# Performance work log

Measured on AMD Instinct MI355X. Metric: run time of the kernel, lower is better.

The kernel has to match this reference:

```python
import jax, jax.numpy as jnp
import numpy as np

B, L, D = 2, 2048, 1024
H, DH = 16, 64            # heads, dim_head; inner_dim = H*DH = 1024
SCALE = DH ** -0.5


def setup_inputs() -> dict:
    key = jax.random.key(0)
    ks = jax.random.split(key, 7)
    s = 0.02
    return {
        "x": jax.random.normal(ks[0], (B, L, D), dtype=jnp.float32),
        "attention_mask": jnp.zeros((B * H, L, L), dtype=jnp.float32),
        "Wq": jax.random.normal(ks[1], (H * DH, D), dtype=jnp.float32) * s,
        "Wk": jax.random.normal(ks[2], (H * DH, D), dtype=jnp.float32) * s,
        "Wv": jax.random.normal(ks[3], (H * DH, D), dtype=jnp.float32) * s,
        "Wo": jax.random.normal(ks[4], (D, H * DH), dtype=jnp.float32) * s,
        "bo": jnp.zeros((D,), dtype=jnp.float32),
    }


def _split_heads(t):
    # [B, L, H*DH] -> [(B*H), L, DH]
    b, l, _ = t.shape
    return t.reshape(b, l, H, DH).transpose(0, 2, 1, 3).reshape(b * H, l, DH)


def reference(x, attention_mask, Wq, Wk, Wv, Wo, bo):
    # Self-attention: encoder_hidden_states = hidden_states
    q = _split_heads(jnp.einsum('bld,ed->ble', x, Wq))  # [(B*H), L, DH]
    k = _split_heads(jnp.einsum('bld,ed->ble', x, Wk))
    v = _split_heads(jnp.einsum('bld,ed->ble', x, Wv))
    # baddbmm: mask + scale * q @ k^T  -> [(B*H), L, L]
    scores = attention_mask + SCALE * jnp.einsum('nqd,nkd->nqk', q, k)
    probs = jax.nn.softmax(scores, axis=-1)
    hidden = jnp.einsum('nqk,nkd->nqd', probs, v)       # [(B*H), L, DH]
    hidden = hidden.reshape(B, H, L, DH).transpose(0, 2, 1, 3).reshape(B, L, H * DH)
    return jnp.einsum('ble,de->bld', hidden, Wo) + bo   # out projection (dropout=0)
```

## Files before the change

kernel.cpp:

```cpp
#include <hip/hip_runtime.h>


typedef __attribute__((ext_vector_type(8))) short short8;
typedef __attribute__((ext_vector_type(8))) __bf16 bf16x8;
typedef __attribute__((ext_vector_type(4))) float f32x4;

#define GLDS16(gp, lp)                                                         \
  __builtin_amdgcn_global_load_lds(                                            \
      (const __attribute__((address_space(1))) void*)(gp),                     \
      (__attribute__((address_space(3))) void*)(lp), 16, 0, 0)

__device__ __forceinline__ unsigned short f2bf(float f) {
  unsigned u = __builtin_bit_cast(unsigned, f);
  u += 0x7fffu + ((u >> 16) & 1u);
  return (unsigned short)(u >> 16);
}

__global__ __launch_bounds__(256) void convert_all(
    const float* __restrict__ x, const float* __restrict__ wq,
    const float* __restrict__ wk, const float* __restrict__ wv,
    const float* __restrict__ wo, unsigned short* __restrict__ xb,
    unsigned short* __restrict__ wqkv, unsigned short* __restrict__ wob) {
  const int X4 = (2 * 2048 * 1024) / 4;
  const int W4 = (1024 * 1024) / 4;
  const int total = X4 + 4 * W4;
  for (int i = blockIdx.x * 256 + threadIdx.x; i < total;
       i += gridDim.x * 256) {
    const float* src; unsigned short* dst; int off;
    if (i < X4)               { src = x;  dst = xb;                   off = i; }
    else if (i < X4 + W4)     { src = wq; dst = wqkv;                 off = i - X4; }
    else if (i < X4 + 2 * W4) { src = wk; dst = wqkv + 1024 * 1024;   off = i - X4 - W4; }
    else if (i < X4 + 3 * W4) { src = wv; dst = wqkv + 2 * 1024 * 1024; off = i - X4 - 2 * W4; }
    else                      { src = wo; dst = wob;                  off = i - X4 - 3 * W4; }
    float4 v = ((const float4*)src)[off];
    uint2 o;
    o.x = (unsigned)f2bf(v.x) | ((unsigned)f2bf(v.y) << 16);
    o.y = (unsigned)f2bf(v.z) | ((unsigned)f2bf(v.w) << 16);
    ((uint2*)dst)[off] = o;
  }
}

template <int MODE>
__global__ __launch_bounds__(256, 2) void gemm_bt(
    const unsigned short* __restrict__ A, const unsigned short* __restrict__ Bw,
    unsigned short* __restrict__ o_q, unsigned short* __restrict__ o_k,
    unsigned short* __restrict__ o_vT, const float* __restrict__ bias,
    float* __restrict__ o_f) {
  constexpr int K = 1024;
  __shared__ unsigned short As[128 * 32];
  __shared__ unsigned short Bs[128 * 32];
  const int t = threadIdx.x;
  const int w = t >> 6;
  const int lane = t & 63;
  const int g = lane >> 4;
  const int q16 = lane & 15;
  const int wm = w >> 1, wn = w & 1;
  const int bn0 = blockIdx.x * 128, bm0 = blockIdx.y * 128;
  const int arow = t >> 2;
  const int acol = (t & 3) * 8;

  f32x4 acc[4][4];
  const f32x4 z4 = {0.f, 0.f, 0.f, 0.f};
#pragma unroll
  for (int i = 0; i < 4; ++i)
#pragma unroll
    for (int j = 0; j < 4; ++j) acc[i][j] = z4;

  for (int k0 = 0; k0 < K; k0 += 32) {
#pragma unroll
    for (int c = 0; c < 2; ++c) {
      GLDS16(A + (size_t)(bm0 + c * 64 + arow) * K + k0 + acol,
             As + c * 2048 + w * 512);
      GLDS16(Bw + (size_t)(bn0 + c * 64 + arow) * K + k0 + acol,
             Bs + c * 2048 + w * 512);
    }
    __syncthreads();
    bf16x8 af[4], bf[4];
#pragma unroll
    for (int i = 0; i < 4; ++i)
      af[i] = *(const bf16x8*)(As + (wm * 64 + i * 16 + q16) * 32 + g * 8);
#pragma unroll
    for (int j = 0; j < 4; ++j)
      bf[j] = *(const bf16x8*)(Bs + (wn * 64 + j * 16 + q16) * 32 + g * 8);
#pragma unroll
    for (int i = 0; i < 4; ++i)
#pragma unroll
      for (int j = 0; j < 4; ++j)
        acc[i][j] =
            __builtin_amdgcn_mfma_f32_16x16x32_bf16(af[i], bf[j], acc[i][j], 0, 0, 0);
    __syncthreads();
  }

  if constexpr (MODE == 0) {
    const int which = bn0 >> 10;
#pragma unroll
    for (int i = 0; i < 4; ++i)
#pragma unroll
      for (int j = 0; j < 4; ++j)
#pragma unroll
        for (int r = 0; r < 4; ++r) {
          const int m = bm0 + wm * 64 + i * 16 + g * 4 + r;
          const int n = (bn0 & 1023) + wn * 64 + j * 16 + q16;
          const float v = acc[i][j][r];
          const int bb = m >> 11, lp = m & 2047;
          const int h = n >> 6, d = n & 63;
          const int bh = bb * 16 + h;
          if (which == 0)
            o_q[((size_t)bh * 2048 + lp) * 64 + d] = f2bf(v * 0.125f);
          else if (which == 1)
            o_k[((size_t)bh * 2048 + lp) * 64 + d] = f2bf(v);
          else
            o_vT[((size_t)bh * 64 + d) * 2048 + lp] = f2bf(v);
        }
  } else {
#pragma unroll
    for (int i = 0; i < 4; ++i)
#pragma unroll
      for (int j = 0; j < 4; ++j)
#pragma unroll
        for (int r = 0; r < 4; ++r) {
          const int m = bm0 + wm * 64 + i * 16 + g * 4 + r;
          const int n = bn0 + wn * 64 + j * 16 + q16;
          o_f[(size_t)m * 1024 + n] = acc[i][j][r] + bias[n];
        }
  }
}

__global__ __launch_bounds__(256, 3) void attn_kernel(
    const unsigned short* __restrict__ kb, const unsigned short* __restrict__ qb,
    const unsigned short* __restrict__ vT, const float* __restrict__ mask,
    unsigned short* __restrict__ hb) {
  __shared__ float Mst[3 * 2048];
  __shared__ unsigned short Kst[3 * 2048];
  __shared__ unsigned short Vst[3 * 2048];
  __shared__ unsigned short Plds[4][16][40];
  const int orig = blockIdx.x;
  const int bid = (orig & 7) * 128 + (orig >> 3);
  const int bh = bid >> 5, qt = bid & 31;
  const int t = threadIdx.x, w = t >> 6, lane = t & 63;
  const int g = lane >> 4, q16 = lane & 15;
  const int qrow0 = qt * 64;
  const int qrow = qrow0 + w * 16;

  const unsigned short* qptr = qb + ((size_t)bh * 2048 + qrow + q16) * 64 + g * 8;
  bf16x8 qf0 = *(const bf16x8*)(qptr);
  bf16x8 qf1 = *(const bf16x8*)(qptr + 32);

  f32x4 O[4];
  const f32x4 z4 = {0.f, 0.f, 0.f, 0.f};
#pragma unroll
  for (int dt = 0; dt < 4; ++dt) O[dt] = z4;
  float mrun = -1e30f, lsum = 0.f;

  const float* mbase = mask + ((size_t)bh * 2048 + qrow0) * 2048;
  const int fA = (w * 2 + 0) * 64 + lane;
  const int fB = (w * 2 + 1) * 64 + lane;
  const int rA = fA >> 3, cA = (fA & 7) ^ (rA & 7);
  const int rB = fB >> 3, cB = (fB & 7) ^ (rB & 7);
  const float* msrcA = mbase + (size_t)rA * 2048 + cA * 4;
  const float* msrcB = mbase + (size_t)rB * 2048 + cB * 4;
  const int rK = w * 8 + (lane >> 3), cK = (lane & 7) ^ (rK & 7);
  const unsigned short* ksrc = kb + (size_t)bh * 2048 * 64 + (size_t)rK * 64 + cK * 8;
  const int rV = w * 16 + (lane >> 2), cV = (lane & 3) ^ ((rV >> 1) & 3);
  const unsigned short* vsrc = vT + (size_t)bh * 64 * 2048 + (size_t)rV * 2048 + cV * 8;

  const int kx0 = (g ^ (q16 & 7)) * 8;
  const int kx1 = ((g + 4) ^ (q16 & 7)) * 8;
  const int mo0 = (w * 16 + q16) * 32 + (g ^ (q16 & 7)) * 4;
  const int mo1 = (w * 16 + q16) * 32 + ((g + 4) ^ (q16 & 7)) * 4;
  const int vx = (g ^ ((q16 >> 1) & 3)) * 8;

#define STAGE(ti)                                                              \
  do {                                                                         \
    const int s_ = (ti) % 3;                                                   \
    const size_t kvb_ = (size_t)((ti) < 64 ? (ti) : 63) * 32;                  \
    GLDS16(ksrc + kvb_ * 64, Kst + s_ * 2048 + w * 512);                       \
    GLDS16(vsrc + kvb_, Vst + s_ * 2048 + w * 512);                            \
    GLDS16(msrcA + kvb_, Mst + s_ * 2048 + (w * 2 + 0) * 256);                 \
    GLDS16(msrcB + kvb_, Mst + s_ * 2048 + (w * 2 + 1) * 256);                 \
  } while (0)

  STAGE(0);
  STAGE(1);
  for (int tl = 0; tl < 64; ++tl) {
    asm volatile("s_waitcnt vmcnt(4)" ::: "memory");
    __builtin_amdgcn_s_barrier();
    __builtin_amdgcn_sched_barrier(0);

    STAGE(tl + 2);

    const int sb = tl % 3;
    const unsigned short* Kb = Kst + sb * 2048;
    const unsigned short* Vb = Vst + sb * 2048;
    const float* Mb = Mst + sb * 2048;

    bf16x8 vf[4];
#pragma unroll
    for (int dt = 0; dt < 4; ++dt)
      vf[dt] = *(const bf16x8*)(Vb + (dt * 16 + q16) * 32 + vx);

    bf16x8 kf0 = *(const bf16x8*)(Kb + q16 * 64 + kx0);
    bf16x8 kf1 = *(const bf16x8*)(Kb + q16 * 64 + kx1);
    bf16x8 kf2 = *(const bf16x8*)(Kb + (16 + q16) * 64 + kx0);
    bf16x8 kf3 = *(const bf16x8*)(Kb + (16 + q16) * 64 + kx1);

    f32x4 S0 = z4, S1 = z4;
    S0 = __builtin_amdgcn_mfma_f32_16x16x32_bf16(kf0, qf0, S0, 0, 0, 0);
    S0 = __builtin_amdgcn_mfma_f32_16x16x32_bf16(kf1, qf1, S0, 0, 0, 0);
    S1 = __builtin_amdgcn_mfma_f32_16x16x32_bf16(kf2, qf0, S1, 0, 0, 0);
    S1 = __builtin_amdgcn_mfma_f32_16x16x32_bf16(kf3, qf1, S1, 0, 0, 0);

    S0 += *(const f32x4*)(Mb + mo0);
    S1 += *(const f32x4*)(Mb + mo1);

    float lmax = fmaxf(fmaxf(fmaxf(S0[0], S0[1]), fmaxf(S0[2], S0[3])),
                       fmaxf(fmaxf(S1[0], S1[1]), fmaxf(S1[2], S1[3])));
    if (!__all(lmax <= mrun + 8.f)) {
      float pm = fmaxf(lmax, __shfl_xor(lmax, 16));
      pm = fmaxf(pm, __shfl_xor(pm, 32));
      const float mnew = fmaxf(mrun, pm);
      const float alpha = __expf(mrun - mnew);
      lsum *= alpha;
      float ar[4];
#pragma unroll
      for (int r = 0; r < 4; ++r) ar[r] = __shfl(alpha, g * 4 + r);
#pragma unroll
      for (int dt = 0; dt < 4; ++dt)
#pragma unroll
        for (int r = 0; r < 4; ++r) O[dt][r] *= ar[r];
      mrun = mnew;
    }

    float p0[4], p1[4], rs = 0.f;
#pragma unroll
    for (int r = 0; r < 4; ++r) {
      p0[r] = __expf(S0[r] - mrun);
      p1[r] = __expf(S1[r] - mrun);
      rs += p0[r] + p1[r];
    }
    lsum += rs;

    uint2 pw0, pw1;
    pw0.x = (unsigned)f2bf(p0[0]) | ((unsigned)f2bf(p0[1]) << 16);
    pw0.y = (unsigned)f2bf(p0[2]) | ((unsigned)f2bf(p0[3]) << 16);
    pw1.x = (unsigned)f2bf(p1[0]) | ((unsigned)f2bf(p1[1]) << 16);
    pw1.y = (unsigned)f2bf(p1[2]) | ((unsigned)f2bf(p1[3]) << 16);
    *(uint2*)&Plds[w][q16][g * 4] = pw0;
    *(uint2*)&Plds[w][q16][16 + g * 4] = pw1;
    bf16x8 pf = *(const bf16x8*)&Plds[w][q16][g * 8];
#pragma unroll
    for (int dt = 0; dt < 4; ++dt)
      O[dt] = __builtin_amdgcn_mfma_f32_16x16x32_bf16(pf, vf[dt], O[dt], 0, 0, 0);
  }
#undef STAGE

  float rsrow = lsum + __shfl_xor(lsum, 16);
  rsrow += __shfl_xor(rsrow, 32);
  float li[4];
#pragma unroll
  for (int r = 0; r < 4; ++r) li[r] = 1.f / __shfl(rsrow, g * 4 + r);
  const int b = bh >> 4, h = bh & 15;
#pragma unroll
  for (int dt = 0; dt < 4; ++dt)
#pragma unroll
    for (int r = 0; r < 4; ++r) {
      const int qg = qrow + g * 4 + r;
      hb[((size_t)b * 2048 + qg) * 1024 + h * 64 + dt * 16 + q16] =
          f2bf(O[dt][r] * li[r]);
    }
}

extern "C" void kernel_launch(void* const* d_in, const int* in_sizes, int n_in,
                              void* d_out, int out_size, void* d_ws,
                              size_t ws_size, hipStream_t stream) {
  const float* x    = (const float*)d_in[0];
  const float* mask = (const float*)d_in[1];
  const float* wq   = (const float*)d_in[2];
  const float* wk   = (const float*)d_in[3];
  const float* wv   = (const float*)d_in[4];
  const float* wo   = (const float*)d_in[5];
  const float* bo   = (const float*)d_in[6];
  float* out = (float*)d_out;
  char* ws = (char*)d_ws;

  unsigned short* xb   = (unsigned short*)(ws);
  unsigned short* wqkv = (unsigned short*)(ws + 8u * 1024 * 1024);
  unsigned short* wob  = (unsigned short*)(ws + 14u * 1024 * 1024);
  unsigned short* qbuf = (unsigned short*)(ws + 16u * 1024 * 1024);
  unsigned short* kbuf = (unsigned short*)(ws + 24u * 1024 * 1024);
  unsigned short* vTb  = (unsigned short*)(ws + 32u * 1024 * 1024);
  unsigned short* hb   = (unsigned short*)(ws + 40u * 1024 * 1024);
  (void)in_sizes; (void)n_in; (void)out_size; (void)ws_size;

  convert_all<<<2048, 256, 0, stream>>>(x, wq, wk, wv, wo, xb, wqkv, wob);
  gemm_bt<0><<<dim3(24, 32), 256, 0, stream>>>(xb, wqkv, qbuf, kbuf, vTb,
                                               nullptr, nullptr);
  attn_kernel<<<1024, 256, 0, stream>>>(kbuf, qbuf, vTb, mask, hb);
  gemm_bt<1><<<dim3(8, 32), 256, 0, stream>>>(hb, wob, nullptr, nullptr,
                                              nullptr, bo, out);
}
```

Measured before the change: 299.7 us.

## Stream attention mask in wide per-row chunks with double-buffered LDS staging

The attention kernel stops fetching the additive mask in 32-float slices per key tile inside the 3-stage ring. Each wave now prefetches its own 16 mask rows in 256-float (1 KB) contiguous chunks covering 8 key tiles, into a double-buffered 2x64x256 float LDS array. Those loads are spread two rows per iteration across the stage, and the vmcnt waits are adjusted so the buffer is complete at each stage boundary. Wider contiguous reads of the large mask should use DRAM more efficiently, but LDS use rises to about 128 KB and launch bounds drop to 1 block per CU, which cuts occupancy and latency hiding.

```diff
diff --git a/kernel.cpp b/kernel.cpp
--- a/kernel.cpp
+++ b/kernel.cpp
@@ -126,11 +126,11 @@
   }
 }
 
-__global__ __launch_bounds__(256, 3) void attn_kernel(
+__global__ __launch_bounds__(256, 1) void attn_kernel(
     const unsigned short* __restrict__ kb, const unsigned short* __restrict__ qb,
     const unsigned short* __restrict__ vT, const float* __restrict__ mask,
     unsigned short* __restrict__ hb) {
-  __shared__ float Mst[3 * 2048];
+  __shared__ float Mst[2][64][256];
   __shared__ unsigned short Kst[3 * 2048];
   __shared__ unsigned short Vst[3 * 2048];
   __shared__ unsigned short Plds[4][16][40];
@@ -152,47 +152,50 @@
   for (int dt = 0; dt < 4; ++dt) O[dt] = z4;
   float mrun = -1e30f, lsum = 0.f;
 
-  const float* mbase = mask + ((size_t)bh * 2048 + qrow0) * 2048;
-  const int fA = (w * 2 + 0) * 64 + lane;
-  const int fB = (w * 2 + 1) * 64 + lane;
-  const int rA = fA >> 3, cA = (fA & 7) ^ (rA & 7);
-  const int rB = fB >> 3, cB = (fB & 7) ^ (rB & 7);
-  const float* msrcA = mbase + (size_t)rA * 2048 + cA * 4;
-  const float* msrcB = mbase + (size_t)rB * 2048 + cB * 4;
   const int rK = w * 8 + (lane >> 3), cK = (lane & 7) ^ (rK & 7);
   const unsigned short* ksrc = kb + (size_t)bh * 2048 * 64 + (size_t)rK * 64 + cK * 8;
   const int rV = w * 16 + (lane >> 2), cV = (lane & 3) ^ ((rV >> 1) & 3);
   const unsigned short* vsrc = vT + (size_t)bh * 64 * 2048 + (size_t)rV * 2048 + cV * 8;
-
-  const int kx0 = (g ^ (q16 & 7)) * 8;
-  const int kx1 = ((g + 4) ^ (q16 & 7)) * 8;
-  const int mo0 = (w * 16 + q16) * 32 + (g ^ (q16 & 7)) * 4;
-  const int mo1 = (w * 16 + q16) * 32 + ((g + 4) ^ (q16 & 7)) * 4;
+  const float* mA = mask + ((size_t)bh * 2048 + qrow0 + w * 16) * 2048;
+  const int la = lane & 56, lb = lane & 7;
+
+  const int x7 = q16 & 7;
+  const int kx0 = (g ^ x7) * 8;
+  const int kx1 = ((g + 4) ^ x7) * 8;
+  const int cg0 = (g ^ x7) * 4;
+  const int cg1 = ((g + 4) ^ x7) * 4;
   const int vx = (g ^ ((q16 >> 1) & 3)) * 8;
 
-#define STAGE(ti)                                                              \
-  do {                                                                         \
-    const int s_ = (ti) % 3;                                                   \
-    const size_t kvb_ = (size_t)((ti) < 64 ? (ti) : 63) * 32;                  \
-    GLDS16(ksrc + kvb_ * 64, Kst + s_ * 2048 + w * 512);                       \
-    GLDS16(vsrc + kvb_, Vst + s_ * 2048 + w * 512);                            \
-    GLDS16(msrcA + kvb_, Mst + s_ * 2048 + (w * 2 + 0) * 256);                 \
-    GLDS16(msrcB + kvb_, Mst + s_ * 2048 + (w * 2 + 1) * 256);                 \
-  } while (0)
-
-  STAGE(0);
-  STAGE(1);
+#pragma unroll
+  for (int j = 0; j < 16; ++j)
+    GLDS16(mA + (size_t)j * 2048 + (la | (lb ^ (j & 7))) * 4, &Mst[0][w * 16 + j][0]);
+  GLDS16(ksrc, Kst + 0 * 2048 + w * 512);
+  GLDS16(vsrc, Vst + 0 * 2048 + w * 512);
+  GLDS16(ksrc + (size_t)1 * 2048, Kst + 1 * 2048 + w * 512);
+  GLDS16(vsrc + (size_t)1 * 32, Vst + 1 * 2048 + w * 512);
+
   for (int tl = 0; tl < 64; ++tl) {
-    asm volatile("s_waitcnt vmcnt(4)" ::: "memory");
+    const int s = tl >> 3, u = tl & 7;
+    if (u == 0) asm volatile("s_waitcnt vmcnt(2)" ::: "memory");
+    else        asm volatile("s_waitcnt vmcnt(4)" ::: "memory");
     __builtin_amdgcn_s_barrier();
     __builtin_amdgcn_sched_barrier(0);
 
-    STAGE(tl + 2);
+    {
+      const int sn = (s + 1 < 8) ? s + 1 : 7;
+      const int r0 = 2 * u, r1 = 2 * u + 1;
+      GLDS16(mA + (size_t)r0 * 2048 + sn * 256 + (la | (lb ^ (r0 & 7))) * 4,
+             &Mst[(s + 1) & 1][w * 16 + r0][0]);
+      GLDS16(mA + (size_t)r1 * 2048 + sn * 256 + (la | (lb ^ (r1 & 7))) * 4,
+             &Mst[(s + 1) & 1][w * 16 + r1][0]);
+      const int tn = (tl + 2 < 64) ? tl + 2 : 63;
+      GLDS16(ksrc + (size_t)tn * 2048, Kst + ((tl + 2) % 3) * 2048 + w * 512);
+      GLDS16(vsrc + (size_t)tn * 32, Vst + ((tl + 2) % 3) * 2048 + w * 512);
+    }
 
     const int sb = tl % 3;
     const unsigned short* Kb = Kst + sb * 2048;
     const unsigned short* Vb = Vst + sb * 2048;
-    const float* Mb = Mst + sb * 2048;
 
     bf16x8 vf[4];
 #pragma unroll
@@ -210,8 +213,11 @@
     S1 = __builtin_amdgcn_mfma_f32_16x16x32_bf16(kf2, qf0, S1, 0, 0, 0);
     S1 = __builtin_amdgcn_mfma_f32_16x16x32_bf16(kf3, qf1, S1, 0, 0, 0);
 
-    S0 += *(const f32x4*)(Mb + mo0);
-    S1 += *(const f32x4*)(Mb + mo1);
+    {
+      const float* Mb = &Mst[s & 1][w * 16 + q16][u * 32];
+      S0 += *(const f32x4*)(Mb + cg0);
+      S1 += *(const f32x4*)(Mb + cg1);
+    }
 
     float lmax = fmaxf(fmaxf(fmaxf(S0[0], S0[1]), fmaxf(S0[2], S0[3])),
                        fmaxf(fmaxf(S1[0], S1[1]), fmaxf(S1[2], S1[3])));
@@ -252,7 +258,6 @@
     for (int dt = 0; dt < 4; ++dt)
       O[dt] = __builtin_amdgcn_mfma_f32_16x16x32_bf16(pf, vf[dt], O[dt], 0, 0, 0);
   }
-#undef STAGE
 
   float rsrow = lsum + __shfl_xor(lsum, 16);
   rsrow += __shfl_xor(rsrow, 32);
```

Measured after the change: 387.4 us. 29.3% more time.
